# Optimization experiments

Hardware: AMD Instinct MI355X
Metric: run time of the kernel (lower is better)

## Reference

```python
import jax, jax.numpy as jnp
import numpy as np

B = 4096
F_ST, F_DY, M = 20, 10, 50
E = 16
N_ST, N_DY = 100000, 1000000
F_ALL = F_ST + F_DY                      # 30 fields total
P = F_ALL * (F_ALL - 1) // 2             # 435 strict upper-triangular pairs
D_IN = P * E                             # 6960 MLP input dim
H = 512
BN_EPS = 1e-5


def _bn(x, g, b):
    # BatchNorm1d in training mode: biased batch variance (matches torch)
    m = jnp.mean(x, axis=0)
    v = jnp.var(x, axis=0)
    return g * (x - m) * jax.lax.rsqrt(v + BN_EPS) + b


def setup_inputs() -> dict:
    key = jax.random.key(0)
    ks = jax.random.split(key, 16)
    s_emb = 0.02
    inp = {
        "static_ids": jax.random.randint(ks[0], (B, F_ST), 0, N_ST),
        "dynamic_ids": jax.random.randint(ks[1], (B, F_DY, M), 0, N_DY),
        "dynamic_lengths": jax.random.randint(ks[2], (B, F_DY), 1, M + 1),
        "st_emb": jax.random.normal(ks[3], (N_ST, E), jnp.float32) * s_emb,
        "dy_emb": jax.random.normal(ks[4], (N_DY, E), jnp.float32) * s_emb,
        "st_lr": jax.random.normal(ks[5], (N_ST, 1), jnp.float32) * s_emb,
        "dy_lr": jax.random.normal(ks[6], (N_DY, 1), jnp.float32) * s_emb,
        "bias": jax.random.normal(ks[7], (1,), jnp.float32),
        "bn1_g": jnp.ones((D_IN,), jnp.float32), "bn1_b": jnp.zeros((D_IN,), jnp.float32),
        "W1": jax.random.normal(ks[8], (D_IN, H), jnp.float32) / np.sqrt(D_IN),
        "b1": jnp.zeros((H,), jnp.float32),
        "bn2_g": jnp.ones((H,), jnp.float32), "bn2_b": jnp.zeros((H,), jnp.float32),
        "W2": jax.random.normal(ks[9], (H, H), jnp.float32) / np.sqrt(H),
        "b2": jnp.zeros((H,), jnp.float32),
        "bn3_g": jnp.ones((H,), jnp.float32), "bn3_b": jnp.zeros((H,), jnp.float32),
        "W3": jax.random.normal(ks[10], (H, H), jnp.float32) / np.sqrt(H),
        "b3": jnp.zeros((H,), jnp.float32),
        "bn_out_g": jnp.ones((H,), jnp.float32), "bn_out_b": jnp.zeros((H,), jnp.float32),
        "W_out": jax.random.normal(ks[11], (H, 1), jnp.float32) / np.sqrt(H),
        "b_out": jnp.zeros((1,), jnp.float32),
    }
    return inp


def reference(static_ids, dynamic_ids, dynamic_lengths,
              st_emb, dy_emb, st_lr, dy_lr, bias,
              bn1_g, bn1_b, W1, b1,
              bn2_g, bn2_b, W2, b2,
              bn3_g, bn3_b, W3, b3,
              bn_out_g, bn_out_b, W_out, b_out):
    lengths = jnp.maximum(dynamic_lengths, 1)                       # guard avg div
    valid = (jnp.arange(M)[None, None, :] < lengths[:, :, None])    # [B,Fdy,M]
    valid_f = valid.astype(jnp.float32)

    # DyEmb (method='avg'): masked mean over list positions -> [B,Fdy,E]
    dyn_tab = dy_emb[dynamic_ids]                                   # [B,Fdy,M,E]
    dyn_embeddings = jnp.einsum('bfme,bfm->bfe', dyn_tab, valid_f) / lengths[..., None].astype(jnp.float32)
    # StEmb: plain lookup -> [B,Fst,E]
    st_embeddings = st_emb[static_ids]

    all_emb = jnp.concatenate([st_embeddings, dyn_embeddings], axis=1)  # [B,F_ALL,E]

    # Strict upper triangle pairs (static indices == the boolean mask in torch code)
    iu, ju = np.triu_indices(F_ALL, k=1)                            # each [P]
    combine = all_emb[:, iu, :] * all_emb[:, ju, :]                 # [B,P,E]
    x = combine.reshape(combine.shape[0], -1)                       # [B, P*E]

    # Linear parts: StEmb/DyEmb with embedding_size=1 (dyLr uses method='sum')
    static_lr_out = st_lr[static_ids][..., 0]                       # [B,Fst]
    dyn_lr_out = jnp.einsum('bfm,bfm->bf', dy_lr[dynamic_ids][..., 0], valid_f)  # [B,Fdy]

    # BN -> Linear -> ReLU tower
    h1 = _bn(x, bn1_g, bn1_b) @ W1 + b1
    h2 = _bn(jax.nn.relu(h1), bn2_g, bn2_b) @ W2 + b2
    out3 = _bn(jax.nn.relu(h2), bn3_g, bn3_b) @ W3 + b3             # embedding_lr_out_3
    # final BN+Linear is computed in torch but unused in scores (kept faithful)
    _ = _bn(jax.nn.relu(out3), bn_out_g, bn_out_b) @ W_out + b_out

    scores = (bias
              + jnp.sum(static_lr_out, axis=-1)
              + jnp.sum(dyn_lr_out, axis=-1)
              + jnp.sum(out3, axis=-1))                             # [B]
    return scores
```

## Files before the change

### kernel.cpp

```cpp
#include <hip/hip_runtime.h>

typedef __attribute__((ext_vector_type(8))) short short8;
typedef __attribute__((ext_vector_type(4))) float f32x4;

__device__ __forceinline__ unsigned short f2b(float f) {
    union { float f; unsigned u; } uf; uf.f = f;
    unsigned r = uf.u + 0x7fffu + ((uf.u >> 16) & 1u);
    return (unsigned short)(r >> 16);
}
__device__ __forceinline__ float b2f(unsigned short b) {
    union { unsigned u; float f; } uf; uf.u = ((unsigned)b) << 16;
    return uf.f;
}
__device__ __forceinline__ void gload_lds16(const void* g, void* l) {
    __builtin_amdgcn_global_load_lds(
        (const __attribute__((address_space(1))) void*)g,
        (__attribute__((address_space(3))) void*)l,
        16, 0, 0);
}

#define B_SZ 4096
#define F_ST 20
#define F_DY 10
#define MLEN 50
#define E_SZ 16
#define F_ALL 30
#define NPAIR 435
#define DIN 6960
#define KP 7168
#define H_SZ 512
#define BN_EPS 1e-5f

__global__ __launch_bounds__(256) void k_stemb(
    const int* __restrict__ st_ids, const float* __restrict__ st_emb,
    float* __restrict__ all_emb)
{
    int idx = blockIdx.x * 256 + threadIdx.x;
    int e4 = idx & 3, bf = idx >> 2;
    int b = bf / F_ST, f = bf % F_ST;
    int id = st_ids[bf];
    f32x4 v = *(const f32x4*)(st_emb + (long)id * E_SZ + e4 * 4);
    *(f32x4*)(all_emb + ((long)b * F_ALL + f) * E_SZ + e4 * 4) = v;
}

__global__ __launch_bounds__(512) void k_dyemb(
    const int* __restrict__ dy_ids, const int* __restrict__ dy_len,
    const float* __restrict__ dy_emb, float* __restrict__ all_emb)
{
    int gw = blockIdx.x * 8 + (threadIdx.x >> 6);
    int l = threadIdx.x & 63;
    int b = gw / F_DY, f = gw - b * F_DY;
    int len = dy_len[b * F_DY + f]; if (len < 1) len = 1;
    const int* ids = dy_ids + ((long)b * F_DY + f) * MLEN;
    int idv = (l < MLEN) ? ids[l] : 0;
    int e = l & 15, mq = l >> 4;
    float acc = 0.f;
#pragma unroll
    for (int j = 0; j < 13; ++j) {
        int m = mq + (j << 2);
        int id = __shfl(idv, m, 64);
        float v = (m < len) ? dy_emb[(long)id * E_SZ + e] : 0.f;
        acc += v;
    }
    acc += __shfl_xor(acc, 16, 64);
    acc += __shfl_xor(acc, 32, 64);
    if (l < 16)
        all_emb[((long)b * F_ALL + F_ST + f) * E_SZ + e] = acc / (float)len;
}

__global__ __launch_bounds__(512) void k_lr(
    const int* __restrict__ st_ids, const int* __restrict__ dy_ids,
    const int* __restrict__ dy_len, const float* __restrict__ st_lr,
    const float* __restrict__ dy_lr, const float* __restrict__ bias,
    float* __restrict__ lr_score)
{
    int w = threadIdx.x >> 6, l = threadIdx.x & 63;
    int b = blockIdx.x * 8 + w;
    float acc = 0.f;
    if (l < F_ST) acc += st_lr[st_ids[b * F_ST + l]];
#pragma unroll
    for (int i = 0; i < 8; ++i) {
        int idx = i * 64 + l;
        if (idx < F_DY * MLEN) {
            int f = idx / MLEN, m = idx - f * MLEN;
            int len = dy_len[b * F_DY + f]; if (len < 1) len = 1;
            if (m < len)
                acc += dy_lr[dy_ids[((long)b * F_DY + f) * MLEN + m]];
        }
    }
    for (int s = 32; s; s >>= 1) acc += __shfl_down(acc, s, 64);
    if (l == 0) lr_score[b] = bias[0] + acc;
}

__global__ __launch_bounds__(256) void k_x(
    const float* __restrict__ all_emb, unsigned short* __restrict__ x16,
    float* __restrict__ s1, float* __restrict__ s1q)
{
    __shared__ float es[16 * 480];
    __shared__ int pip[NPAIR], pjp[NPAIR];
    int t = threadIdx.x, b0 = blockIdx.x * 16;
    for (int p = t; p < NPAIR; p += 256) {
        int i = 0, rem = p;
        while (rem >= (F_ALL - 1) - i) { rem -= (F_ALL - 1) - i; ++i; }
        pip[p] = i; pjp[p] = i + 1 + rem;
    }
    for (int idx = t; idx < 16 * 480; idx += 256)
        es[idx] = all_emb[(long)b0 * 480 + idx];
    __syncthreads();

    int ci[28], cj[28];
#pragma unroll
    for (int k = 0; k < 28; ++k) {
        int d = t + (k << 8);
        if (d < DIN) {
            int p = d >> 4, e = d & 15;
            ci[k] = pip[p] * E_SZ + e;
            cj[k] = pjp[p] * E_SZ + e;
        } else { ci[k] = -1; cj[k] = 0; }
    }
    float sum[28], sq[28];
#pragma unroll
    for (int k = 0; k < 28; ++k) { sum[k] = 0.f; sq[k] = 0.f; }

    for (int r = 0; r < 16; ++r) {
        const float* row = &es[r * 480];
        long ob = (long)(b0 + r) * KP;
#pragma unroll
        for (int k = 0; k < 28; ++k) {
            int d = t + (k << 8);
            if (ci[k] >= 0) {
                float v = row[ci[k]] * row[cj[k]];
                unsigned short h = f2b(v);
                x16[ob + d] = h;
                float vb = b2f(h);
                sum[k] += vb; sq[k] += vb * vb;
            } else {
                x16[ob + d] = 0;
            }
        }
    }
#pragma unroll
    for (int k = 0; k < 28; ++k) {
        int d = t + (k << 8);
        if (ci[k] >= 0) { atomicAdd(&s1[d], sum[k]); atomicAdd(&s1q[d], sq[k]); }
    }
}

__global__ __launch_bounds__(256) void k_prep(
    const float* __restrict__ s, const float* __restrict__ sqs,
    const float* __restrict__ g, const float* __restrict__ bb,
    float* __restrict__ a, float* __restrict__ c,
    const float* __restrict__ W3, float* __restrict__ w3s)
{
    int t = threadIdx.x;
    if (blockIdx.x < 28) {
        int d = blockIdx.x * 256 + t;
        if (d < DIN) {
            float m = s[d] * (1.f / 4096.f);
            float var = sqs[d] * (1.f / 4096.f) - m * m;
            float av = g[d] * rsqrtf(var + BN_EPS);
            a[d] = av; c[d] = bb[d] - m * av;
        }
    } else {
        int row = (blockIdx.x - 28) * 16 + (t >> 4), sub = t & 15;
        float acc = 0.f;
        for (int i = 0; i < 32; ++i) acc += W3[(long)row * H_SZ + sub + i * 16];
#pragma unroll
        for (int sh = 8; sh; sh >>= 1) acc += __shfl_xor(acc, sh, 16);
        if (sub == 0) w3s[row] = acc;
    }
}

__global__ __launch_bounds__(256) void k_w1t(
    const float* __restrict__ W1, const float* __restrict__ a1,
    const float* __restrict__ c1, unsigned short* __restrict__ w1t,
    float* __restrict__ con)
{
    int gi = blockIdx.x * 256 + threadIdx.x;
    int kg = gi >> 9, n = gi & 511;
    short8 out; float cacc = 0.f;
#pragma unroll
    for (int i = 0; i < 8; ++i) {
        int k = kg * 8 + i;
        if (k < DIN) {
            float w = W1[(long)k * H_SZ + n];
            out[i] = (short)f2b(a1[k] * w);
            cacc += c1[k] * w;
        } else out[i] = 0;
    }
    *(short8*)(w1t + (long)n * KP + kg * 8) = out;
    atomicAdd(&con[n], cacc);
}

__global__ __launch_bounds__(512, 2) void k_gemm1(
    const unsigned short* __restrict__ A, const unsigned short* __restrict__ Bt,
    float* __restrict__ accbuf)
{
    __shared__ __align__(16) short As[64 * 64];
    __shared__ __align__(16) short Bs[512 * 64];
    const int t = threadIdx.x;
    const int w = t >> 6, l = t & 63;
    const int lm = l & 15, lq = l >> 4;
    const int s = blockIdx.x;
    const int row0 = (s >> 3) * 64;
    const int k0 = (s & 7) * (KP / 8);

    const int srow = t >> 3;
    const int gch = (t & 7) ^ (srow & 7);
    const unsigned short* gA = A + (long)(row0 + srow) * KP + k0 + gch * 8;
    const unsigned short* gB = Bt + (long)srow * KP + k0 + gch * 8;
    short* AsW = As + w * 512;
    short* BsW = Bs + w * 512;

    f32x4 acc[4][4];
#pragma unroll
    for (int mi = 0; mi < 4; ++mi)
#pragma unroll
        for (int ni = 0; ni < 4; ++ni) acc[mi][ni] = (f32x4){0.f,0.f,0.f,0.f};

    for (int kt = 0; kt < 14; ++kt) {
        gload_lds16(gA, AsW);
#pragma unroll
        for (int c = 0; c < 8; ++c)
            gload_lds16(gB + (long)(64 * c) * KP, BsW + c * 4096);
        __syncthreads();
#pragma unroll
        for (int s2 = 0; s2 < 2; ++s2) {
            short8 af[4];
#pragma unroll
            for (int mi = 0; mi < 4; ++mi) {
                int m = mi * 16 + lm;
                int sl = (s2 * 4 + lq) ^ (m & 7);
                af[mi] = *(const short8*)(As + m * 64 + sl * 8);
            }
#pragma unroll
            for (int ni = 0; ni < 4; ++ni) {
                int rb = w * 64 + ni * 16 + lm;
                int sl = (s2 * 4 + lq) ^ (rb & 7);
                short8 bf = *(const short8*)(Bs + rb * 64 + sl * 8);
#pragma unroll
                for (int mi = 0; mi < 4; ++mi)
                    acc[mi][ni] = __builtin_amdgcn_mfma_f32_16x16x32_bf16(
                        af[mi], bf, acc[mi][ni], 0, 0, 0);
            }
        }
        __syncthreads();
        gA += 64; gB += 64;
    }

#pragma unroll
    for (int ni = 0; ni < 4; ++ni) {
        int col = w * 64 + ni * 16 + lm;
#pragma unroll
        for (int mi = 0; mi < 4; ++mi) {
            int rbase = row0 + mi * 16 + lq * 4;
#pragma unroll
            for (int r = 0; r < 4; ++r)
                atomicAdd(&accbuf[(long)(rbase + r) * H_SZ + col], acc[mi][ni][r]);
        }
    }
}

__global__ __launch_bounds__(256) void k_ep(
    const float* __restrict__ accbuf, const float* __restrict__ con1,
    const float* __restrict__ b1, unsigned short* __restrict__ r1,
    float* __restrict__ s2, float* __restrict__ s2q)
{
    __shared__ float con[H_SZ];
    int t = threadIdx.x, r0 = blockIdx.x * 32;
    con[t] = b1[t] + con1[t];
    con[t + 256] = b1[t + 256] + con1[t + 256];
    __syncthreads();
    float a0 = 0.f, q0 = 0.f, a1v = 0.f, q1 = 0.f;
    for (int r = 0; r < 32; ++r) {
        long base = (long)(r0 + r) * H_SZ;
        float v0 = accbuf[base + t] + con[t];
        float v1 = accbuf[base + t + 256] + con[t + 256];
        v0 = v0 > 0.f ? v0 : 0.f;
        v1 = v1 > 0.f ? v1 : 0.f;
        unsigned short h0 = f2b(v0), h1 = f2b(v1);
        r1[base + t] = h0; r1[base + t + 256] = h1;
        float b0 = b2f(h0), b1f = b2f(h1);
        a0 += b0; q0 += b0 * b0; a1v += b1f; q1 += b1f * b1f;
    }
    atomicAdd(&s2[t], a0);        atomicAdd(&s2q[t], q0);
    atomicAdd(&s2[t + 256], a1v); atomicAdd(&s2q[t + 256], q1);
}

__global__ __launch_bounds__(256) void k_w2t(
    const float* __restrict__ W2, const float* __restrict__ s2,
    const float* __restrict__ s2q, const float* __restrict__ g2,
    const float* __restrict__ bb2, unsigned short* __restrict__ w2t,
    float* __restrict__ con)
{
    int gi = blockIdx.x * 256 + threadIdx.x;
    int kg = gi >> 9, n = gi & 511;
    short8 out; float cacc = 0.f;
#pragma unroll
    for (int i = 0; i < 8; ++i) {
        int k = kg * 8 + i;
        float m = s2[k] * (1.f / 4096.f);
        float var = s2q[k] * (1.f / 4096.f) - m * m;
        float av = g2[k] * rsqrtf(var + BN_EPS);
        float cv = bb2[k] - m * av;
        float w = W2[(long)k * H_SZ + n];
        out[i] = (short)f2b(av * w);
        cacc += cv * w;
    }
    *(short8*)(w2t + (long)n * H_SZ + kg * 8) = out;
    atomicAdd(&con[n], cacc);
}

__global__ __launch_bounds__(512) void k_gemm2(
    const unsigned short* __restrict__ A, const unsigned short* __restrict__ Bt,
    const float* __restrict__ cvec, const float* __restrict__ bvec,
    unsigned short* __restrict__ Out, float* __restrict__ ss,
    float* __restrict__ sq)
{
    const int Kp = H_SZ;
    __shared__ __align__(16) short As[128 * 32];
    __shared__ __align__(16) short Bs[64 * 32];
    const int t = threadIdx.x;
    const int w = t >> 6, l = t & 63;
    const int wm = w >> 1, wn = w & 1;
    const int lm = l & 15, lq = l >> 4;
    const int row0 = blockIdx.y * 128;
    const int col0 = blockIdx.x * 64;

    const unsigned short* gA = A + (long)(row0 + (t >> 2)) * Kp + ((t & 3) * 8);
    const unsigned short* gB = Bt + (long)(col0 + ((t >> 2) & 63)) * Kp + ((t & 3) * 8);
    short* AsW = As + w * 512;
    short* BsW = Bs + w * 512;

    const short* aBase0 = As + (wm * 32 + lm) * 32 + lq * 8;
    const short* aBase1 = aBase0 + 16 * 32;
    const short* bBase0 = Bs + (wn * 32 + lm) * 32 + lq * 8;
    const short* bBase1 = bBase0 + 16 * 32;

    f32x4 acc00 = {0.f,0.f,0.f,0.f}, acc01 = acc00, acc10 = acc00, acc11 = acc00;

    for (int kt = 0; kt < Kp / 32; ++kt) {
        gload_lds16(gA, AsW);
        if (t < 256) gload_lds16(gB, BsW);
        __syncthreads();
        short8 af0 = *(const short8*)aBase0;
        short8 af1 = *(const short8*)aBase1;
        short8 bf0 = *(const short8*)bBase0;
        short8 bf1 = *(const short8*)bBase1;
        acc00 = __builtin_amdgcn_mfma_f32_16x16x32_bf16(af0, bf0, acc00, 0, 0, 0);
        acc01 = __builtin_amdgcn_mfma_f32_16x16x32_bf16(af0, bf1, acc01, 0, 0, 0);
        acc10 = __builtin_amdgcn_mfma_f32_16x16x32_bf16(af1, bf0, acc10, 0, 0, 0);
        acc11 = __builtin_amdgcn_mfma_f32_16x16x32_bf16(af1, bf1, acc11, 0, 0, 0);
        __syncthreads();
        gA += 32; gB += 32;
    }

    f32x4 accs[2][2] = {{acc00, acc01}, {acc10, acc11}};
#pragma unroll
    for (int ni = 0; ni < 2; ++ni) {
        int col = col0 + wn * 32 + ni * 16 + lm;
        float cb = cvec[col] + bvec[col];
        float psum = 0.f, psq = 0.f;
#pragma unroll
        for (int mi = 0; mi < 2; ++mi) {
            int rbase = row0 + wm * 32 + mi * 16 + lq * 4;
#pragma unroll
            for (int r = 0; r < 4; ++r) {
                float v = accs[mi][ni][r] + cb;
                v = v > 0.f ? v : 0.f;
                unsigned short h = f2b(v);
                Out[(long)(rbase + r) * H_SZ + col] = h;
                float vb = b2f(h);
                psum += vb; psq += vb * vb;
            }
        }
        psum += __shfl_xor(psum, 16, 64); psum += __shfl_xor(psum, 32, 64);
        psq  += __shfl_xor(psq , 16, 64); psq  += __shfl_xor(psq , 32, 64);
        if (lq == 0) { atomicAdd(&ss[col], psum); atomicAdd(&sq[col], psq); }
    }
}

__global__ __launch_bounds__(256) void k_final(
    const unsigned short* __restrict__ r2, const float* __restrict__ s3,
    const float* __restrict__ s3q, const float* __restrict__ g3,
    const float* __restrict__ bb3, const float* __restrict__ w3s,
    const float* __restrict__ b3, const float* __restrict__ lr_score,
    float* __restrict__ out)
{
    int t = threadIdx.x, w = t >> 6, l = t & 63;
    int b = blockIdx.x * 4 + w;
    float acc = 0.f;
#pragma unroll
    for (int i = 0; i < 8; ++i) {
        int e = i * 64 + l;
        float m = s3[e] * (1.f / 4096.f);
        float var = s3q[e] * (1.f / 4096.f) - m * m;
        float a3 = g3[e] * rsqrtf(var + BN_EPS);
        float c3 = bb3[e] - m * a3;
        float v = a3 * b2f(r2[(long)b * H_SZ + e]) + c3;
        acc += v * w3s[e] + b3[e];
    }
    for (int s = 32; s; s >>= 1) acc += __shfl_down(acc, s, 64);
    if (l == 0) out[b] = lr_score[b] + acc;
}

extern "C" void kernel_launch(void* const* d_in, const int* in_sizes, int n_in,
                              void* d_out, int out_size, void* d_ws, size_t ws_size,
                              hipStream_t stream) {
    const int*   st_ids = (const int*)d_in[0];
    const int*   dy_ids = (const int*)d_in[1];
    const int*   dy_len = (const int*)d_in[2];
    const float* st_emb = (const float*)d_in[3];
    const float* dy_emb = (const float*)d_in[4];
    const float* st_lr  = (const float*)d_in[5];
    const float* dy_lr  = (const float*)d_in[6];
    const float* bias   = (const float*)d_in[7];
    const float* bn1_g  = (const float*)d_in[8];
    const float* bn1_b  = (const float*)d_in[9];
    const float* W1     = (const float*)d_in[10];
    const float* b1     = (const float*)d_in[11];
    const float* bn2_g  = (const float*)d_in[12];
    const float* bn2_b  = (const float*)d_in[13];
    const float* W2     = (const float*)d_in[14];
    const float* b2     = (const float*)d_in[15];
    const float* bn3_g  = (const float*)d_in[16];
    const float* bn3_b  = (const float*)d_in[17];
    const float* W3     = (const float*)d_in[18];
    const float* b3     = (const float*)d_in[19];

    char* ws = (char*)d_ws;
    size_t off = 0;
    auto alloc = [&](size_t bytes) -> char* {
        char* p = ws + off;
        off = (off + bytes + 255) & ~(size_t)255;
        return p;
    };
    char* R = alloc((size_t)B_SZ * H_SZ * 4);
    float*          all_emb = (float*)R;
    float*          accbuf  = (float*)R;
    unsigned short* r2      = (unsigned short*)R;

    unsigned short* x16     = (unsigned short*)alloc((size_t)B_SZ * KP * 2);
    unsigned short* w1t     = (unsigned short*)alloc((size_t)H_SZ * KP * 2);
    unsigned short* r1      = (unsigned short*)alloc((size_t)B_SZ * H_SZ * 2);
    unsigned short* w2t     = (unsigned short*)alloc((size_t)H_SZ * H_SZ * 2);
    float*          lr_sc   = (float*)alloc(B_SZ * 4);
    float* a1  = (float*)alloc(KP * 4);
    float* c1  = (float*)alloc(KP * 4);
    float* w3s = (float*)alloc(H_SZ * 4);
    char* zstart = ws + off;
    float* s1   = (float*)alloc(KP * 4);
    float* s1q  = (float*)alloc(KP * 4);
    float* con1 = (float*)alloc(H_SZ * 4);
    float* s2   = (float*)alloc(H_SZ * 4);
    float* s2q  = (float*)alloc(H_SZ * 4);
    float* con2 = (float*)alloc(H_SZ * 4);
    float* s3   = (float*)alloc(H_SZ * 4);
    float* s3q  = (float*)alloc(H_SZ * 4);
    size_t zbytes = (size_t)((ws + off) - zstart);

    hipMemsetAsync(zstart, 0, zbytes, stream);
    k_stemb<<<(B_SZ * F_ST * 4) / 256, 256, 0, stream>>>(st_ids, st_emb, all_emb);
    k_dyemb<<<(B_SZ * F_DY) / 8, 512, 0, stream>>>(dy_ids, dy_len, dy_emb, all_emb);
    k_lr<<<B_SZ / 8, 512, 0, stream>>>(st_ids, dy_ids, dy_len, st_lr, dy_lr,
                                       bias, lr_sc);
    k_x<<<B_SZ / 16, 256, 0, stream>>>(all_emb, x16, s1, s1q);
    hipMemsetAsync(R, 0, (size_t)B_SZ * H_SZ * 4, stream);
    k_prep<<<60, 256, 0, stream>>>(s1, s1q, bn1_g, bn1_b, a1, c1, W3, w3s);
    k_w1t<<<(896 * 512) / 256, 256, 0, stream>>>(W1, a1, c1, w1t, con1);
    k_gemm1<<<512, 512, 0, stream>>>(x16, w1t, accbuf);
    k_ep<<<128, 256, 0, stream>>>(accbuf, con1, b1, r1, s2, s2q);
    k_w2t<<<128, 256, 0, stream>>>(W2, s2, s2q, bn2_g, bn2_b, w2t, con2);
    k_gemm2<<<dim3(8, 32), 512, 0, stream>>>(r1, w2t, con2, b2, r2, s3, s3q);
    k_final<<<B_SZ / 4, 256, 0, stream>>>(r2, s3, s3q, bn3_g, bn3_b, w3s, b3,
                                          lr_sc, (float*)d_out);
}
```

Measured before the change: 389.2 us.

## Double-buffer LDS in both GEMMs and enlarge gemm1 row tile

Both GEMM kernels now keep two LDS buffers and prefetch the next K-slice while computing on the current one, removing one barrier per iteration. gemm1 also doubles its row tile to 128, halving the grid and reusing each B tile across twice as many rows. The cost is much larger LDS use (about 160 KB in gemm1) and twice the accumulator registers. This likely limits gemm1 to one block per CU, reducing latency hiding and conflicting with its launch bound of 2.

```diff
diff --git a/kernel.cpp b/kernel.cpp
--- a/kernel.cpp
+++ b/kernel.cpp
@@ -196,69 +196,77 @@
     const unsigned short* __restrict__ A, const unsigned short* __restrict__ Bt,
     float* __restrict__ accbuf)
 {
-    __shared__ __align__(16) short As[64 * 64];
-    __shared__ __align__(16) short Bs[512 * 64];
+    __shared__ __align__(16) short As[2][128 * 64];
+    __shared__ __align__(16) short Bs[2][512 * 64];
     const int t = threadIdx.x;
     const int w = t >> 6, l = t & 63;
     const int lm = l & 15, lq = l >> 4;
     const int s = blockIdx.x;
-    const int row0 = (s >> 3) * 64;
+    const int row0 = (s >> 3) * 128;
     const int k0 = (s & 7) * (KP / 8);
 
     const int srow = t >> 3;
     const int gch = (t & 7) ^ (srow & 7);
     const unsigned short* gA = A + (long)(row0 + srow) * KP + k0 + gch * 8;
     const unsigned short* gB = Bt + (long)srow * KP + k0 + gch * 8;
-    short* AsW = As + w * 512;
-    short* BsW = Bs + w * 512;
-
-    f32x4 acc[4][4];
-#pragma unroll
-    for (int mi = 0; mi < 4; ++mi)
+
+    f32x4 acc[8][4];
+#pragma unroll
+    for (int mi = 0; mi < 8; ++mi)
 #pragma unroll
         for (int ni = 0; ni < 4; ++ni) acc[mi][ni] = (f32x4){0.f,0.f,0.f,0.f};
 
+#define STAGE1(kt, pb) do {                                                   \
+        const unsigned short* a_ = gA + (kt) * 64;                            \
+        const unsigned short* b_ = gB + (kt) * 64;                            \
+        gload_lds16(a_, &As[pb][w * 512]);                   \
+        gload_lds16(a_ + (long)64 * KP, &As[pb][4096 + w * 512]); \
+        _Pragma("unroll")                                                     \
+        for (int c_ = 0; c_ < 8; ++c_)                       \
+            gload_lds16(b_ + (long)(64 * c_) * KP, &Bs[pb][c_ * 4096 + w * 512]); \
+    } while (0)
+
+    STAGE1(0, 0);
+    __syncthreads();
+
     for (int kt = 0; kt < 14; ++kt) {
-        gload_lds16(gA, AsW);
-#pragma unroll
-        for (int c = 0; c < 8; ++c)
-            gload_lds16(gB + (long)(64 * c) * KP, BsW + c * 4096);
-        __syncthreads();
-#pragma unroll
-        for (int s2 = 0; s2 < 2; ++s2) {
-            short8 af[4];
-#pragma unroll
-            for (int mi = 0; mi < 4; ++mi) {
+        const int pb = kt & 1;
+        if (kt < 13) STAGE1(kt + 1, pb ^ 1);
+#pragma unroll
+        for (int sb = 0; sb < 2; ++sb) {
+            short8 af[8];
+#pragma unroll
+            for (int mi = 0; mi < 8; ++mi) {
                 int m = mi * 16 + lm;
-                int sl = (s2 * 4 + lq) ^ (m & 7);
-                af[mi] = *(const short8*)(As + m * 64 + sl * 8);
+                int sl = (sb * 4 + lq) ^ (m & 7);
+                af[mi] = *(const short8*)(&As[pb][m * 64 + sl * 8]);
             }
 #pragma unroll
             for (int ni = 0; ni < 4; ++ni) {
                 int rb = w * 64 + ni * 16 + lm;
-                int sl = (s2 * 4 + lq) ^ (rb & 7);
-                short8 bf = *(const short8*)(Bs + rb * 64 + sl * 8);
-#pragma unroll
-                for (int mi = 0; mi < 4; ++mi)
+                int sl = (sb * 4 + lq) ^ (rb & 7);
+                short8 bf = *(const short8*)(&Bs[pb][rb * 64 + sl * 8]);
+#pragma unroll
+                for (int mi = 0; mi < 8; ++mi)
                     acc[mi][ni] = __builtin_amdgcn_mfma_f32_16x16x32_bf16(
                         af[mi], bf, acc[mi][ni], 0, 0, 0);
             }
         }
         __syncthreads();
-        gA += 64; gB += 64;
     }
 
 #pragma unroll
     for (int ni = 0; ni < 4; ++ni) {
         int col = w * 64 + ni * 16 + lm;
 #pragma unroll
-        for (int mi = 0; mi < 4; ++mi) {
+        for (int mi = 0; mi < 8; ++mi) {
             int rbase = row0 + mi * 16 + lq * 4;
 #pragma unroll
             for (int r = 0; r < 4; ++r)
                 atomicAdd(&accbuf[(long)(rbase + r) * H_SZ + col], acc[mi][ni][r]);
         }
     }
+#undef STAGE1
 }
 
 __global__ __launch_bounds__(256) void k_ep(
@@ -318,8 +326,8 @@
     float* __restrict__ sq)
 {
     const int Kp = H_SZ;
-    __shared__ __align__(16) short As[128 * 32];
-    __shared__ __align__(16) short Bs[64 * 32];
+    __shared__ __align__(16) short As[2][128 * 32];
+    __shared__ __align__(16) short Bs[2][64 * 32];
     const int t = threadIdx.x;
     const int w = t >> 6, l = t & 63;
     const int wm = w >> 1, wn = w & 1;
@@ -329,31 +337,33 @@
 
     const unsigned short* gA = A + (long)(row0 + (t >> 2)) * Kp + ((t & 3) * 8);
     const unsigned short* gB = Bt + (long)(col0 + ((t >> 2) & 63)) * Kp + ((t & 3) * 8);
-    short* AsW = As + w * 512;
-    short* BsW = Bs + w * 512;
-
-    const short* aBase0 = As + (wm * 32 + lm) * 32 + lq * 8;
-    const short* aBase1 = aBase0 + 16 * 32;
-    const short* bBase0 = Bs + (wn * 32 + lm) * 32 + lq * 8;
-    const short* bBase1 = bBase0 + 16 * 32;
+
+#define STAGE2(kt, pb) do {                                                   \
+        gload_lds16(gA + (kt) * 32, &As[pb][w * 512]);                        \
+        if (t < 256) gload_lds16(gB + (kt) * 32, &Bs[pb][w * 512]);           \
+    } while (0)
 
     f32x4 acc00 = {0.f,0.f,0.f,0.f}, acc01 = acc00, acc10 = acc00, acc11 = acc00;
 
+    STAGE2(0, 0);
+    __syncthreads();
+
     for (int kt = 0; kt < Kp / 32; ++kt) {
-        gload_lds16(gA, AsW);
-        if (t < 256) gload_lds16(gB, BsW);
-        __syncthreads();
+        const int pb = kt & 1;
+        if (kt < Kp / 32 - 1) STAGE2(kt + 1, pb ^ 1);
+        const short* aBase0 = &As[pb][(wm * 32 + lm) * 32 + lq * 8];
+        const short* bBase0 = &Bs[pb][(wn * 32 + lm) * 32 + lq * 8];
         short8 af0 = *(const short8*)aBase0;
-        short8 af1 = *(const short8*)aBase1;
+        short8 af1 = *(const short8*)(aBase0 + 16 * 32);
         short8 bf0 = *(const short8*)bBase0;
-        short8 bf1 = *(const short8*)bBase1;
+        short8 bf1 = *(const short8*)(bBase0 + 16 * 32);
         acc00 = __builtin_amdgcn_mfma_f32_16x16x32_bf16(af0, bf0, acc00, 0, 0, 0);
         acc01 = __builtin_amdgcn_mfma_f32_16x16x32_bf16(af0, bf1, acc01, 0, 0, 0);
         acc10 = __builtin_amdgcn_mfma_f32_16x16x32_bf16(af1, bf0, acc10, 0, 0, 0);
         acc11 = __builtin_amdgcn_mfma_f32_16x16x32_bf16(af1, bf1, acc11, 0, 0, 0);
         __syncthreads();
-        gA += 32; gB += 32;
-    }
+    }
+#undef STAGE2
 
     f32x4 accs[2][2] = {{acc00, acc01}, {acc10, acc11}};
 #pragma unroll
@@ -468,7 +478,7 @@
     hipMemsetAsync(R, 0, (size_t)B_SZ * H_SZ * 4, stream);
     k_prep<<<60, 256, 0, stream>>>(s1, s1q, bn1_g, bn1_b, a1, c1, W3, w3s);
     k_w1t<<<(896 * 512) / 256, 256, 0, stream>>>(W1, a1, c1, w1t, con1);
-    k_gemm1<<<512, 512, 0, stream>>>(x16, w1t, accbuf);
+    k_gemm1<<<256, 512, 0, stream>>>(x16, w1t, accbuf);
     k_ep<<<128, 256, 0, stream>>>(accbuf, con1, b1, r1, s2, s2q);
     k_w2t<<<128, 256, 0, stream>>>(W2, s2, s2q, bn2_g, bn2_b, w2t, con2);
     k_gemm2<<<dim3(8, 32), 512, 0, stream>>>(r1, w2t, con2, b2, r2, s3, s3q);
```

After: 396.2 us. No clear change (+1.8%).

## Fuse embedding gathers, LR sum and pair products into one front kernel; double-buffer gemm2

Applied to the files above, without the earlier changes.

Merges the static/dynamic embedding gathers, the linear-term sums and the pairwise-product kernel into a single 512-thread kernel. The gathered embeddings are built directly in shared memory, so the all_emb round trip through global memory and three kernel launches go away. Separately, gemm2 gets double-buffered LDS so the next K tile loads while the current one is multiplied. The cost is more per-block work in the front kernel, shared-memory atomics for the LR sum, and possibly lower occupancy during the gather phase.

```diff
diff --git a/kernel.cpp b/kernel.cpp
--- a/kernel.cpp
+++ b/kernel.cpp
@@ -31,103 +31,93 @@
 #define H_SZ 512
 #define BN_EPS 1e-5f
 
-__global__ __launch_bounds__(256) void k_stemb(
-    const int* __restrict__ st_ids, const float* __restrict__ st_emb,
-    float* __restrict__ all_emb)
-{
-    int idx = blockIdx.x * 256 + threadIdx.x;
-    int e4 = idx & 3, bf = idx >> 2;
-    int b = bf / F_ST, f = bf % F_ST;
-    int id = st_ids[bf];
-    f32x4 v = *(const f32x4*)(st_emb + (long)id * E_SZ + e4 * 4);
-    *(f32x4*)(all_emb + ((long)b * F_ALL + f) * E_SZ + e4 * 4) = v;
-}
-
-__global__ __launch_bounds__(512) void k_dyemb(
-    const int* __restrict__ dy_ids, const int* __restrict__ dy_len,
-    const float* __restrict__ dy_emb, float* __restrict__ all_emb)
-{
-    int gw = blockIdx.x * 8 + (threadIdx.x >> 6);
-    int l = threadIdx.x & 63;
-    int b = gw / F_DY, f = gw - b * F_DY;
-    int len = dy_len[b * F_DY + f]; if (len < 1) len = 1;
-    const int* ids = dy_ids + ((long)b * F_DY + f) * MLEN;
-    int idv = (l < MLEN) ? ids[l] : 0;
-    int e = l & 15, mq = l >> 4;
-    float acc = 0.f;
-#pragma unroll
-    for (int j = 0; j < 13; ++j) {
-        int m = mq + (j << 2);
-        int id = __shfl(idv, m, 64);
-        float v = (m < len) ? dy_emb[(long)id * E_SZ + e] : 0.f;
-        acc += v;
-    }
-    acc += __shfl_xor(acc, 16, 64);
-    acc += __shfl_xor(acc, 32, 64);
-    if (l < 16)
-        all_emb[((long)b * F_ALL + F_ST + f) * E_SZ + e] = acc / (float)len;
-}
-
-__global__ __launch_bounds__(512) void k_lr(
+__global__ __launch_bounds__(512) void k_front(
     const int* __restrict__ st_ids, const int* __restrict__ dy_ids,
-    const int* __restrict__ dy_len, const float* __restrict__ st_lr,
-    const float* __restrict__ dy_lr, const float* __restrict__ bias,
-    float* __restrict__ lr_score)
-{
-    int w = threadIdx.x >> 6, l = threadIdx.x & 63;
-    int b = blockIdx.x * 8 + w;
-    float acc = 0.f;
-    if (l < F_ST) acc += st_lr[st_ids[b * F_ST + l]];
-#pragma unroll
-    for (int i = 0; i < 8; ++i) {
-        int idx = i * 64 + l;
-        if (idx < F_DY * MLEN) {
-            int f = idx / MLEN, m = idx - f * MLEN;
-            int len = dy_len[b * F_DY + f]; if (len < 1) len = 1;
-            if (m < len)
-                acc += dy_lr[dy_ids[((long)b * F_DY + f) * MLEN + m]];
-        }
-    }
-    for (int s = 32; s; s >>= 1) acc += __shfl_down(acc, s, 64);
-    if (l == 0) lr_score[b] = bias[0] + acc;
-}
-
-__global__ __launch_bounds__(256) void k_x(
-    const float* __restrict__ all_emb, unsigned short* __restrict__ x16,
-    float* __restrict__ s1, float* __restrict__ s1q)
+    const int* __restrict__ dy_len,
+    const float* __restrict__ st_emb, const float* __restrict__ dy_emb,
+    const float* __restrict__ st_lr, const float* __restrict__ dy_lr,
+    const float* __restrict__ bias,
+    unsigned short* __restrict__ x16, float* __restrict__ s1,
+    float* __restrict__ s1q, float* __restrict__ lr_sc)
 {
     __shared__ float es[16 * 480];
     __shared__ int pip[NPAIR], pjp[NPAIR];
-    int t = threadIdx.x, b0 = blockIdx.x * 16;
-    for (int p = t; p < NPAIR; p += 256) {
-        int i = 0, rem = p;
+    __shared__ float lrs[16];
+    const int t = threadIdx.x;
+    const int w = t >> 6, l = t & 63;
+    const int b0 = blockIdx.x * 16;
+
+    if (t < 16) lrs[t] = bias[0];
+    if (t < NPAIR) {
+        int i = 0, rem = t;
         while (rem >= (F_ALL - 1) - i) { rem -= (F_ALL - 1) - i; ++i; }
-        pip[p] = i; pjp[p] = i + 1 + rem;
-    }
-    for (int idx = t; idx < 16 * 480; idx += 256)
-        es[idx] = all_emb[(long)b0 * 480 + idx];
+        pip[t] = i; pjp[t] = i + 1 + rem;
+    }
     __syncthreads();
 
-    int ci[28], cj[28];
-#pragma unroll
-    for (int k = 0; k < 28; ++k) {
-        int d = t + (k << 8);
+    for (int i = t; i < 16 * F_ST * 4; i += 512) {
+        int e4 = i & 3, bf = i >> 2;
+        int r = bf / F_ST, f = bf - r * F_ST;
+        int id = st_ids[(b0 + r) * F_ST + f];
+        f32x4 v = *(const f32x4*)(st_emb + (long)id * E_SZ + e4 * 4);
+        *(f32x4*)(&es[r * 480 + f * 16 + e4 * 4]) = v;
+    }
+    if (t < 16 * F_ST) {
+        int r = t / F_ST, f = t - r * F_ST;
+        atomicAdd(&lrs[r], st_lr[st_ids[(b0 + r) * F_ST + f]]);
+    }
+
+    {
+        int e = l & 15, mq = l >> 4;
+        for (int pi = 0; pi < 20; ++pi) {
+            int pair = pi * 8 + w;
+            int r = pair / F_DY, f = pair - r * F_DY;
+            int b = b0 + r;
+            int len = dy_len[b * F_DY + f]; if (len < 1) len = 1;
+            const int* ids = dy_ids + ((long)b * F_DY + f) * MLEN;
+            int idv = (l < MLEN) ? ids[l] : 0;
+            float acc = 0.f, lac = 0.f;
+#pragma unroll
+            for (int j = 0; j < 13; ++j) {
+                int m = mq + (j << 2);
+                int id = __shfl(idv, m, 64);
+                bool p = (m < len);
+                float v = p ? dy_emb[(long)id * E_SZ + e] : 0.f;
+                acc += v;
+                if (e == 0) lac += p ? dy_lr[id] : 0.f;
+            }
+            acc += __shfl_xor(acc, 16, 64);
+            acc += __shfl_xor(acc, 32, 64);
+            lac += __shfl_xor(lac, 16, 64);
+            lac += __shfl_xor(lac, 32, 64);
+            if (l == 0) atomicAdd(&lrs[r], lac);
+            if (l < 16)
+                es[r * 480 + (F_ST + f) * 16 + e] = acc / (float)len;
+        }
+    }
+    __syncthreads();
+    if (t < 16) lr_sc[b0 + t] = lrs[t];
+
+    int ci[14], cj[14];
+#pragma unroll
+    for (int k = 0; k < 14; ++k) {
+        int d = t + (k << 9);
         if (d < DIN) {
             int p = d >> 4, e = d & 15;
             ci[k] = pip[p] * E_SZ + e;
             cj[k] = pjp[p] * E_SZ + e;
         } else { ci[k] = -1; cj[k] = 0; }
     }
-    float sum[28], sq[28];
-#pragma unroll
-    for (int k = 0; k < 28; ++k) { sum[k] = 0.f; sq[k] = 0.f; }
+    float sum[14], sq[14];
+#pragma unroll
+    for (int k = 0; k < 14; ++k) { sum[k] = 0.f; sq[k] = 0.f; }
 
     for (int r = 0; r < 16; ++r) {
         const float* row = &es[r * 480];
         long ob = (long)(b0 + r) * KP;
 #pragma unroll
-        for (int k = 0; k < 28; ++k) {
-            int d = t + (k << 8);
+        for (int k = 0; k < 14; ++k) {
+            int d = t + (k << 9);
             if (ci[k] >= 0) {
                 float v = row[ci[k]] * row[cj[k]];
                 unsigned short h = f2b(v);
@@ -140,8 +130,8 @@
         }
     }
 #pragma unroll
-    for (int k = 0; k < 28; ++k) {
-        int d = t + (k << 8);
+    for (int k = 0; k < 14; ++k) {
+        int d = t + (k << 9);
         if (ci[k] >= 0) { atomicAdd(&s1[d], sum[k]); atomicAdd(&s1q[d], sq[k]); }
     }
 }
@@ -225,18 +215,18 @@
             gload_lds16(gB + (long)(64 * c) * KP, BsW + c * 4096);
         __syncthreads();
 #pragma unroll
-        for (int s2 = 0; s2 < 2; ++s2) {
+        for (int sb = 0; sb < 2; ++sb) {
             short8 af[4];
 #pragma unroll
             for (int mi = 0; mi < 4; ++mi) {
                 int m = mi * 16 + lm;
-                int sl = (s2 * 4 + lq) ^ (m & 7);
+                int sl = (sb * 4 + lq) ^ (m & 7);
                 af[mi] = *(const short8*)(As + m * 64 + sl * 8);
             }
 #pragma unroll
             for (int ni = 0; ni < 4; ++ni) {
                 int rb = w * 64 + ni * 16 + lm;
-                int sl = (s2 * 4 + lq) ^ (rb & 7);
+                int sl = (sb * 4 + lq) ^ (rb & 7);
                 short8 bf = *(const short8*)(Bs + rb * 64 + sl * 8);
 #pragma unroll
                 for (int mi = 0; mi < 4; ++mi)
@@ -318,8 +308,8 @@
     float* __restrict__ sq)
 {
     const int Kp = H_SZ;
-    __shared__ __align__(16) short As[128 * 32];
-    __shared__ __align__(16) short Bs[64 * 32];
+    __shared__ __align__(16) short As[2][128 * 32];
+    __shared__ __align__(16) short Bs[2][64 * 32];
     const int t = threadIdx.x;
     const int w = t >> 6, l = t & 63;
     const int wm = w >> 1, wn = w & 1;
@@ -329,31 +319,33 @@
 
     const unsigned short* gA = A + (long)(row0 + (t >> 2)) * Kp + ((t & 3) * 8);
     const unsigned short* gB = Bt + (long)(col0 + ((t >> 2) & 63)) * Kp + ((t & 3) * 8);
-    short* AsW = As + w * 512;
-    short* BsW = Bs + w * 512;
-
-    const short* aBase0 = As + (wm * 32 + lm) * 32 + lq * 8;
-    const short* aBase1 = aBase0 + 16 * 32;
-    const short* bBase0 = Bs + (wn * 32 + lm) * 32 + lq * 8;
-    const short* bBase1 = bBase0 + 16 * 32;
+
+#define STAGE2(kt, pb) do {                                                   \
+        gload_lds16(gA + (kt) * 32, &As[pb][w * 512]);                        \
+        if (t < 256) gload_lds16(gB + (kt) * 32, &Bs[pb][w * 512]);           \
+    } while (0)
 
     f32x4 acc00 = {0.f,0.f,0.f,0.f}, acc01 = acc00, acc10 = acc00, acc11 = acc00;
 
+    STAGE2(0, 0);
+    __syncthreads();
+
     for (int kt = 0; kt < Kp / 32; ++kt) {
-        gload_lds16(gA, AsW);
-        if (t < 256) gload_lds16(gB, BsW);
-        __syncthreads();
+        const int pb = kt & 1;
+        if (kt < Kp / 32 - 1) STAGE2(kt + 1, pb ^ 1);
+        const short* aBase0 = &As[pb][(wm * 32 + lm) * 32 + lq * 8];
+        const short* bBase0 = &Bs[pb][(wn * 32 + lm) * 32 + lq * 8];
         short8 af0 = *(const short8*)aBase0;
-        short8 af1 = *(const short8*)aBase1;
+        short8 af1 = *(const short8*)(aBase0 + 16 * 32);
         short8 bf0 = *(const short8*)bBase0;
-        short8 bf1 = *(const short8*)bBase1;
+        short8 bf1 = *(const short8*)(bBase0 + 16 * 32);
         acc00 = __builtin_amdgcn_mfma_f32_16x16x32_bf16(af0, bf0, acc00, 0, 0, 0);
         acc01 = __builtin_amdgcn_mfma_f32_16x16x32_bf16(af0, bf1, acc01, 0, 0, 0);
         acc10 = __builtin_amdgcn_mfma_f32_16x16x32_bf16(af1, bf0, acc10, 0, 0, 0);
         acc11 = __builtin_amdgcn_mfma_f32_16x16x32_bf16(af1, bf1, acc11, 0, 0, 0);
         __syncthreads();
-        gA += 32; gB += 32;
-    }
+    }
+#undef STAGE2
 
     f32x4 accs[2][2] = {{acc00, acc01}, {acc10, acc11}};
 #pragma unroll
@@ -436,7 +428,6 @@
         return p;
     };
     char* R = alloc((size_t)B_SZ * H_SZ * 4);
-    float*          all_emb = (float*)R;
     float*          accbuf  = (float*)R;
     unsigned short* r2      = (unsigned short*)R;
 
@@ -460,12 +451,10 @@
     size_t zbytes = (size_t)((ws + off) - zstart);
 
     hipMemsetAsync(zstart, 0, zbytes, stream);
-    k_stemb<<<(B_SZ * F_ST * 4) / 256, 256, 0, stream>>>(st_ids, st_emb, all_emb);
-    k_dyemb<<<(B_SZ * F_DY) / 8, 512, 0, stream>>>(dy_ids, dy_len, dy_emb, all_emb);
-    k_lr<<<B_SZ / 8, 512, 0, stream>>>(st_ids, dy_ids, dy_len, st_lr, dy_lr,
-                                       bias, lr_sc);
-    k_x<<<B_SZ / 16, 256, 0, stream>>>(all_emb, x16, s1, s1q);
     hipMemsetAsync(R, 0, (size_t)B_SZ * H_SZ * 4, stream);
+    k_front<<<B_SZ / 16, 512, 0, stream>>>(st_ids, dy_ids, dy_len,
+                                           st_emb, dy_emb, st_lr, dy_lr, bias,
+                                           x16, s1, s1q, lr_sc);
     k_prep<<<60, 256, 0, stream>>>(s1, s1q, bn1_g, bn1_b, a1, c1, W3, w3s);
     k_w1t<<<(896 * 512) / 256, 256, 0, stream>>>(W1, a1, c1, w1t, con1);
     k_gemm1<<<512, 512, 0, stream>>>(x16, w1t, accbuf);
```

Measured after the change: 415.5 us. +6.8%, slower.
